# Performance work log

Hardware: AMD Instinct MI355X
Metric: run time of the kernel (lower is better)

The kernel has to match this reference:

```python
import jax, jax.numpy as jnp
import numpy as np
from jax import lax

NUM_CLASSES = 80
LAMBDA_BOX = 5.0   # lambda_coord
LAMBDA_OBJ = 1.0
LAMBDA_CLS = 1.0
SIMOTA_TOPK = 10
EPS = 1e-8


def _pairwise_iou(a, b):
    # a: [G,4], b: [N,4], boxes in x1,y1,x2,y2 -> [G,N]
    lt = jnp.maximum(a[:, None, :2], b[None, :, :2])
    rb = jnp.minimum(a[:, None, 2:], b[None, :, 2:])
    wh = jnp.clip(rb - lt, 0.0)
    inter = wh[..., 0] * wh[..., 1]
    area_a = jnp.clip(a[:, 2] - a[:, 0], 0.0) * jnp.clip(a[:, 3] - a[:, 1], 0.0)
    area_b = jnp.clip(b[:, 2] - b[:, 0], 0.0) * jnp.clip(b[:, 3] - b[:, 1], 0.0)
    return inter / (area_a[:, None] + area_b[None, :] - inter + EPS)


def _elem_iou(a, b):
    # a, b: [N,4] -> [N]
    lt = jnp.maximum(a[:, :2], b[:, :2])
    rb = jnp.minimum(a[:, 2:], b[:, 2:])
    wh = jnp.clip(rb - lt, 0.0)
    inter = wh[:, 0] * wh[:, 1]
    area_a = jnp.clip(a[:, 2] - a[:, 0], 0.0) * jnp.clip(a[:, 3] - a[:, 1], 0.0)
    area_b = jnp.clip(b[:, 2] - b[:, 0], 0.0) * jnp.clip(b[:, 3] - b[:, 1], 0.0)
    return inter / (area_a + area_b - inter + EPS)


def _bce_logits(x, y):
    # elementwise BCEWithLogits: softplus(x) - x*y  (== max(x,0)-x*y+log(1+exp(-|x|)))
    return jax.nn.softplus(x) - x * y


def _per_image(pred, gt_boxes, gt_labels):
    # pred: [N, 5+C]; gt_boxes: [G,4]; gt_labels: [G]
    N = pred.shape[0]
    G = gt_boxes.shape[0]
    C = NUM_CLASSES
    boxes_pred = pred[:, :4]
    obj_pred = pred[:, 4]
    cls_pred = pred[:, 5:]

    # ---- SimOTA matching (YOLOX-style) ----
    ious = _pairwise_iou(gt_boxes, boxes_pred)                 # [G,N]
    onehot = jax.nn.one_hot(gt_labels, C, dtype=pred.dtype)    # [G,C]
    # pairwise BCE cls cost: sum_c softplus(x_nc) - sum_c x_nc * y_gc
    sp_sum = jax.nn.softplus(cls_pred).sum(-1)                 # [N]
    pair_cls = sp_sum[None, :] - onehot @ cls_pred.T           # [G,N]
    cost = pair_cls + 3.0 * (-jnp.log(ious + EPS))             # [G,N]

    topk_ious, _ = lax.top_k(ious, SIMOTA_TOPK)                # [G,10]
    dynamic_ks = jnp.clip(topk_ious.sum(-1), 1.0, None).astype(jnp.int32)  # [G]

    # rank of each anchor in ascending cost order per gt
    ranks = jnp.argsort(jnp.argsort(cost, axis=1), axis=1)     # [G,N]
    matching = ranks < dynamic_ks[:, None]                     # [G,N] bool

    # conflict resolution: anchors matched to >1 gt keep only min-cost gt
    multi = matching.sum(0) > 1                                # [N]
    best_gt = jnp.argmin(cost, axis=0)                         # [N]
    keep = jax.nn.one_hot(best_gt, G, dtype=bool).T            # [G,N]
    matching = jnp.where(multi[None, :], matching & keep, matching)

    fg_mask = matching.any(0)                                  # [N]
    matched_gt_inds = matching.argmax(0)                       # [N]

    # ---- losses (means over fg, computed with masks) ----
    fg_f = fg_mask.astype(pred.dtype)
    nfg = jnp.maximum(fg_f.sum(), 1.0)

    agt_boxes = gt_boxes[matched_gt_inds]                      # [N,4]
    agt_labels = gt_labels[matched_gt_inds]                    # [N]

    d = boxes_pred - agt_boxes
    ad = jnp.abs(d)
    sl1 = jnp.where(ad < 1.0, 0.5 * d * d, ad - 0.5)
    box_loss = (sl1 * fg_f[:, None]).sum() / (nfg * 4.0)

    iou_t = lax.stop_gradient(_elem_iou(boxes_pred, agt_boxes))  # [N]
    obj_s = jax.nn.sigmoid(obj_pred)                             # note: original applies sigmoid then BCEWithLogits
    obj_loss = (_bce_logits(obj_s, iou_t) * fg_f).sum() / nfg

    cls_t = jax.nn.one_hot(agt_labels, C, dtype=pred.dtype)
    cls_loss = (_bce_logits(cls_pred, cls_t) * fg_f[:, None]).sum() / (nfg * C)

    return box_loss, obj_loss, cls_loss


def setup_inputs() -> dict:
    key = jax.random.key(0)
    k1, k2, k3 = jax.random.split(key, 3)
    B, A, H, W = 16, 3, 128, 128
    G = 60
    preds = jax.random.normal(k1, (B, A, H, W, 5 + NUM_CLASSES), dtype=jnp.float32)
    r = jax.random.uniform(k2, (B, G, 4), dtype=jnp.float32)
    xy = r[..., :2] * 100.0
    wh = r[..., 2:] * 20.0 + 1.0
    gt_boxes = jnp.concatenate([xy, xy + wh], axis=-1)
    gt_labels = jax.random.randint(k3, (B, G), 0, NUM_CLASSES, dtype=jnp.int32)
    return {"preds": preds, "gt_boxes": gt_boxes, "gt_labels": gt_labels}


def reference(preds, gt_boxes, gt_labels):
    B, A, H, W, D = preds.shape
    pred = preds[:, 0].reshape(B, H * W, D)
    bl, ol, cl = jax.vmap(_per_image)(pred, gt_boxes, gt_labels)
    box_loss = bl.sum()
    obj_loss = ol.sum()
    cls_loss = cl.sum()
    total = (LAMBDA_BOX * box_loss + LAMBDA_OBJ * obj_loss + LAMBDA_CLS * cls_loss) / B
    return total, box_loss / B, obj_loss / B, cls_loss / B
```

## Files before the change

kernel.cpp:

```cpp
#include <hip/hip_runtime.h>
#include <math.h>

#define BN 16
#define NA 16384
#define NG 60
#define NC 80
#define ND 85

__device__ __forceinline__ float softplusf(float x){
  return log1pf(expf(-fabsf(x))) + fmaxf(x, 0.0f);
}

__global__ __launch_bounds__(256) void k_prep(const float* __restrict__ preds,
    const int* __restrict__ gt_labels, float4* __restrict__ bx,
    float* __restrict__ spsum, float* __restrict__ objp, float* __restrict__ clsg)
{
  __shared__ float4 tilev[64*ND/4];
  __shared__ int lab[NG];
  __shared__ float psum[256];
  float* tile = (float*)tilev;
  const int t = threadIdx.x;
  const int blk = blockIdx.x;
  const int b = blk >> 8;
  const int n0 = (blk & 255) << 6;
  const float4* srcv = (const float4*)(preds + ((size_t)b*3*NA + n0)*ND);
  for (int i = t; i < 1360; i += 256) tilev[i] = srcv[i];
  if (t < NG) lab[t] = gt_labels[b*NG + t];
  __syncthreads();
  const int a = t & 63, q = t >> 6;
  float p = 0.f;
  #pragma unroll
  for (int c = 0; c < 20; c++) p += softplusf(tile[a*ND + 5 + q*20 + c]);
  psum[t] = p;
  __syncthreads();
  const size_t nb = (size_t)b*NA + n0;
  if (t < 64){
    float sp = psum[t] + psum[64+t] + psum[128+t] + psum[192+t];
    spsum[nb + t] = sp;
    bx[nb + t] = make_float4(tile[t*ND+0], tile[t*ND+1], tile[t*ND+2], tile[t*ND+3]);
    objp[nb + t] = tile[t*ND+4];
  }
  #pragma unroll
  for (int r = 0; r < 15; r++){
    int g = q*15 + r;
    clsg[(((size_t)b*NG + g) << 14) + n0 + a] = tile[a*ND + 5 + lab[g]];
  }
}

__global__ __launch_bounds__(256) void k_select(const float* __restrict__ gt_boxes,
    const float4* __restrict__ bx, const float* __restrict__ spsum,
    const float* __restrict__ clsg, int* __restrict__ matched, int* __restrict__ cnt)
{
  const int bid = blockIdx.x;
  const int g = bid >> 4, b = bid & 15;
  const int t = threadIdx.x;
  const int lane = t & 63, w = t >> 6;
  const float* gtp = gt_boxes + (b*NG + g)*4;
  const float gx1 = gtp[0], gy1 = gtp[1], gx2 = gtp[2], gy2 = gtp[3];
  const float garea = fmaxf(gx2-gx1,0.f)*fmaxf(gy2-gy1,0.f);
  const size_t nb = (size_t)b*NA;
  const float* clsrow = clsg + (((size_t)b*NG + g) << 14);

  float il[10];
  float cl[10]; int ci[10];
  #pragma unroll
  for (int j=0;j<10;j++){ il[j] = -1.f; cl[j] = INFINITY; ci[j] = 0x7fffffff; }

  for (int i = t; i < NA; i += 256){
    float4 bb = bx[nb + i];
    float parea = fmaxf(bb.z-bb.x,0.f)*fmaxf(bb.w-bb.y,0.f);
    float ix = fmaxf(fminf(gx2,bb.z)-fmaxf(gx1,bb.x), 0.f);
    float iy = fmaxf(fminf(gy2,bb.w)-fmaxf(gy1,bb.y), 0.f);
    float inter = ix*iy;
    float iou = inter/(garea + parea - inter + 1e-8f);
    float cost = spsum[nb+i] - clsrow[i] + 3.0f*(-logf(iou + 1e-8f));
    if (__any(iou > il[9])){
      float v = iou;
      #pragma unroll
      for (int j=0;j<10;j++){ bool c = v > il[j]; float o = il[j]; il[j]=c?v:o; v=c?o:v; }
    }
    if (__any((cost < cl[9]) || (cost == cl[9] && i < ci[9]))){
      float cv = cost; int ca = i;
      #pragma unroll
      for (int j=0;j<10;j++){
        bool c = (cv < cl[j]) || (cv == cl[j] && ca < ci[j]);
        float ov = cl[j]; int oa = ci[j];
        cl[j] = c?cv:ov; ci[j] = c?ca:oa;
        cv = c?ov:cv;    ca = c?oa:ca;
      }
    }
  }

  __shared__ float wv[4]; __shared__ int wa[4]; __shared__ int ww[4];
  __shared__ float bs10; __shared__ int bwin; __shared__ int bk;

  float s10 = 0.f;
  for (int r = 0; r < 10; r++){
    float v = il[0]; int who = t;
    #pragma unroll
    for (int off = 32; off; off >>= 1){
      float ov = __shfl_xor(v, off);
      int   ow = __shfl_xor(who, off);
      if (ov > v || (ov == v && ow < who)){ v = ov; who = ow; }
    }
    if (lane == 0){ wv[w] = v; ww[w] = who; }
    __syncthreads();
    if (t == 0){
      float bv = wv[0]; int bw = ww[0];
      for (int u=1; u<4; u++) if (wv[u] > bv || (wv[u]==bv && ww[u]<bw)){ bv=wv[u]; bw=ww[u]; }
      s10 += bv; bwin = bw;
    }
    __syncthreads();
    if (t == bwin){
      #pragma unroll
      for (int j=0;j<9;j++) il[j] = il[j+1];
      il[9] = -1.f;
    }
    __syncthreads();
  }
  if (t == 0) bk = (int)fmaxf(s10, 1.0f);
  __syncthreads();
  const int k = bk;

  for (int r = 0; r < k; r++){
    float v = cl[0]; int a = ci[0]; int who = t;
    #pragma unroll
    for (int off = 32; off; off >>= 1){
      float ov = __shfl_xor(v, off);
      int   oa = __shfl_xor(a, off);
      int   ow = __shfl_xor(who, off);
      if (ov < v || (ov == v && (oa < a || (oa == a && ow < who)))){ v=ov; a=oa; who=ow; }
    }
    if (lane == 0){ wv[w] = v; wa[w] = a; ww[w] = who; }
    __syncthreads();
    if (t == 0){
      float bv = wv[0]; int ba = wa[0]; int bw = ww[0];
      for (int u=1; u<4; u++) if (wv[u] < bv || (wv[u]==bv && wa[u] < ba)){ bv=wv[u]; ba=wa[u]; bw=ww[u]; }
      matched[bid*10 + r] = ba; bwin = bw;
    }
    __syncthreads();
    if (t == bwin){
      #pragma unroll
      for (int j=0;j<9;j++){ cl[j] = cl[j+1]; ci[j] = ci[j+1]; }
      cl[9] = INFINITY; ci[9] = 0x7fffffff;
    }
    __syncthreads();
  }
  if (t == 0) cnt[bid] = k;
}

__device__ __forceinline__ float blockSum(float v, float* red, int t){
  red[t] = v; __syncthreads();
  #pragma unroll
  for (int s = 128; s > 0; s >>= 1){
    if (t < s) red[t] += red[t+s];
    __syncthreads();
  }
  float r = red[0]; __syncthreads();
  return r;
}

__global__ __launch_bounds__(256) void k_loss(const float* __restrict__ gt_boxes,
    const int* __restrict__ matched, const int* __restrict__ cnt,
    const float4* __restrict__ bx, const float* __restrict__ spsum,
    const float* __restrict__ objp, const float* __restrict__ clsg,
    float* __restrict__ partials)
{
  __shared__ int lists[NG*10];
  __shared__ int cnts[NG];
  __shared__ float gtb[NG][4];
  __shared__ float red[256];
  const int b = blockIdx.x;
  const int t = threadIdx.x;
  for (int i = t; i < NG*10; i += 256){
    int g = i/10, j = i - g*10;
    lists[i] = matched[(g*16 + b)*10 + j];
  }
  if (t < NG){
    cnts[t] = cnt[t*16 + b];
    float4 gg = ((const float4*)gt_boxes)[b*NG + t];
    gtb[t][0]=gg.x; gtb[t][1]=gg.y; gtb[t][2]=gg.z; gtb[t][3]=gg.w;
  }
  __syncthreads();
  for (int i = t; i < NG*10; i += 256){
    int g = i/10, j = i - g*10;
    if (j >= cnts[g]) lists[i] = -1;
  }
  __syncthreads();

  float boxs = 0.f, objs = 0.f, clss = 0.f, nfg = 0.f;
  const size_t nb = (size_t)b*NA;
  for (int s = t; s < NG*10; s += 256){
    int n = lists[s];
    if (n < 0) continue;
    int g = s/10;
    int m = 0, firstg = -1;
    for (int gp = 0; gp < NG; gp++){
      bool mem = false;
      #pragma unroll
      for (int jp = 0; jp < 10; jp++) mem |= (lists[gp*10 + jp] == n);
      if (mem){ m++; if (firstg < 0) firstg = gp; }
    }
    if (g != firstg) continue;
    float4 bb = bx[nb + n];
    float sp = spsum[nb + n];
    int mg = g;
    if (m > 1){
      float parea = fmaxf(bb.z-bb.x,0.f)*fmaxf(bb.w-bb.y,0.f);
      float best = INFINITY; int bg = 0;
      for (int gp = 0; gp < NG; gp++){
        float ga = fmaxf(gtb[gp][2]-gtb[gp][0],0.f)*fmaxf(gtb[gp][3]-gtb[gp][1],0.f);
        float ix = fmaxf(fminf(gtb[gp][2],bb.z)-fmaxf(gtb[gp][0],bb.x),0.f);
        float iy = fmaxf(fminf(gtb[gp][3],bb.w)-fmaxf(gtb[gp][1],bb.y),0.f);
        float inter = ix*iy;
        float iou = inter/(ga + parea - inter + 1e-8f);
        float c = sp - clsg[(((size_t)b*NG + gp) << 14) + n] + 3.0f*(-logf(iou + 1e-8f));
        if (c < best){ best = c; bg = gp; }
      }
      bool mem = false;
      #pragma unroll
      for (int jp = 0; jp < 10; jp++) mem |= (lists[bg*10 + jp] == n);
      if (!mem) continue;
      mg = bg;
    }
    float gx1=gtb[mg][0], gy1=gtb[mg][1], gx2=gtb[mg][2], gy2=gtb[mg][3];
    float d0=bb.x-gx1, d1=bb.y-gy1, d2=bb.z-gx2, d3=bb.w-gy2;
    float a0=fabsf(d0), a1=fabsf(d1), a2=fabsf(d2), a3=fabsf(d3);
    float sl = (a0<1.f ? 0.5f*d0*d0 : a0-0.5f)
             + (a1<1.f ? 0.5f*d1*d1 : a1-0.5f)
             + (a2<1.f ? 0.5f*d2*d2 : a2-0.5f)
             + (a3<1.f ? 0.5f*d3*d3 : a3-0.5f);
    float parea = fmaxf(bb.z-bb.x,0.f)*fmaxf(bb.w-bb.y,0.f);
    float garea = fmaxf(gx2-gx1,0.f)*fmaxf(gy2-gy1,0.f);
    float ix = fmaxf(fminf(gx2,bb.z)-fmaxf(gx1,bb.x),0.f);
    float iy = fmaxf(fminf(gy2,bb.w)-fmaxf(gy1,bb.y),0.f);
    float inter = ix*iy;
    float iou_t = inter/(parea + garea - inter + 1e-8f);
    float ob = objp[nb + n];
    float sg = 1.f/(1.f + expf(-ob));
    float obce = softplusf(sg) - sg*iou_t;
    float clsb = sp - clsg[(((size_t)b*NG + mg) << 14) + n];
    boxs += sl; objs += obce; clss += clsb; nfg += 1.f;
  }
  float tb = blockSum(boxs, red, t);
  float to = blockSum(objs, red, t);
  float tc = blockSum(clss, red, t);
  float tn = blockSum(nfg,  red, t);
  if (t == 0){
    partials[b*4+0] = tb; partials[b*4+1] = to;
    partials[b*4+2] = tc; partials[b*4+3] = tn;
  }
}

__global__ void k_final(const float* __restrict__ partials, float* __restrict__ out){
  if (threadIdx.x == 0 && blockIdx.x == 0){
    float tb=0.f, to=0.f, tc=0.f;
    for (int b = 0; b < BN; b++){
      float nf = fmaxf(partials[b*4+3], 1.f);
      tb += partials[b*4+0] / (nf * 4.f);
      to += partials[b*4+1] / nf;
      tc += partials[b*4+2] / (nf * (float)NC);
    }
    out[0] = (5.f*tb + to + tc) / (float)BN;
    out[1] = tb / (float)BN;
    out[2] = to / (float)BN;
    out[3] = tc / (float)BN;
  }
}

extern "C" void kernel_launch(void* const* d_in, const int* in_sizes, int n_in,
                              void* d_out, int out_size, void* d_ws, size_t ws_size,
                              hipStream_t stream)
{
  (void)in_sizes; (void)n_in; (void)out_size; (void)ws_size;
  const float* preds     = (const float*)d_in[0];
  const float* gt_boxes  = (const float*)d_in[1];
  const int*   gt_labels = (const int*)d_in[2];
  float* out = (float*)d_out;

  char* ws = (char*)d_ws;
  float4* bx    = (float4*)ws;
  float*  spsum = (float*)(ws + (size_t)BN*NA*sizeof(float4));
  float*  objp  = spsum + (size_t)BN*NA;
  float*  clsg  = objp  + (size_t)BN*NA;
  int* matched  = (int*)(clsg + (size_t)BN*NG*NA);
  int* cnt      = matched + BN*NG*10;
  float* partials = (float*)(cnt + BN*NG);

  k_prep  <<<BN*NA/64, 256, 0, stream>>>(preds, gt_labels, bx, spsum, objp, clsg);
  k_select<<<BN*NG,    256, 0, stream>>>(gt_boxes, bx, spsum, clsg, matched, cnt);
  k_loss  <<<BN,       256, 0, stream>>>(gt_boxes, matched, cnt, bx, spsum, objp, clsg, partials);
  k_final <<<1, 64, 0, stream>>>(partials, out);
}
```

Baseline: 526.6 us.

## Fuse prep and selection into one tiled scan with per-slab top-k merge

Replaces the prep kernel, which materialised per-gt class logits (clsg, about 63 MB), and the per-gt selection kernel with one scan kernel. Each block loads a tile of anchors into shared memory once, computes softplus sums, and evaluates all 60 gts against it. It keeps per-thread top-10 IoU and cost lists, reduces them within 16-lane groups per slab, and a small merge kernel combines the slab candidates. The loss kernel now recomputes softplus sums and class logits directly from preds. Fast-math intrinsics replace the precise exp and log, and the tie-break on equal cost in the insertion is loosened, which may slightly change matching.

```diff
diff --git a/kernel.cpp b/kernel.cpp
--- a/kernel.cpp
+++ b/kernel.cpp
@@ -6,124 +6,185 @@
 #define NG 60
 #define NC 80
 #define ND 85
-
-__device__ __forceinline__ float softplusf(float x){
-  return log1pf(expf(-fabsf(x))) + fmaxf(x, 0.0f);
-}
-
-__global__ __launch_bounds__(256) void k_prep(const float* __restrict__ preds,
-    const int* __restrict__ gt_labels, float4* __restrict__ bx,
-    float* __restrict__ spsum, float* __restrict__ objp, float* __restrict__ clsg)
+#define SLABS 16
+#define SLAB 1024
+#define TILE 128
+#define NTILES 8
+#define GSLOT 64
+
+__device__ __forceinline__ float softplus_fast(float x){
+  return __logf(1.0f + __expf(-fabsf(x))) + fmaxf(x, 0.0f);
+}
+
+__global__ __launch_bounds__(1024) void f_scan(
+    const float* __restrict__ preds, const float* __restrict__ gt_boxes,
+    const int* __restrict__ gt_labels, float* __restrict__ mlist)
 {
-  __shared__ float4 tilev[64*ND/4];
-  __shared__ int lab[NG];
-  __shared__ float psum[256];
+  __shared__ float4 tilev[TILE*ND/4];
+  __shared__ float sp[TILE];
+  __shared__ float4 gtb4[GSLOT];
+  __shared__ float gar[GSLOT];
+  __shared__ int   lab[GSLOT];
   float* tile = (float*)tilev;
   const int t = threadIdx.x;
-  const int blk = blockIdx.x;
-  const int b = blk >> 8;
-  const int n0 = (blk & 255) << 6;
-  const float4* srcv = (const float4*)(preds + ((size_t)b*3*NA + n0)*ND);
-  for (int i = t; i < 1360; i += 256) tilev[i] = srcv[i];
-  if (t < NG) lab[t] = gt_labels[b*NG + t];
+  const int b = blockIdx.x >> 4;
+  const int slab = blockIdx.x & 15;
+
+  if (t < GSLOT){
+    float4 gg = make_float4(0.f,0.f,0.f,0.f);
+    int lb = 0;
+    if (t < NG){ gg = ((const float4*)gt_boxes)[b*NG + t]; lb = gt_labels[b*NG + t]; }
+    gtb4[t] = gg; lab[t] = lb;
+    gar[t] = fmaxf(gg.z-gg.x,0.f)*fmaxf(gg.w-gg.y,0.f);
+  }
   __syncthreads();
-  const int a = t & 63, q = t >> 6;
-  float p = 0.f;
-  #pragma unroll
-  for (int c = 0; c < 20; c++) p += softplusf(tile[a*ND + 5 + q*20 + c]);
-  psum[t] = p;
-  __syncthreads();
-  const size_t nb = (size_t)b*NA + n0;
-  if (t < 64){
-    float sp = psum[t] + psum[64+t] + psum[128+t] + psum[192+t];
-    spsum[nb + t] = sp;
-    bx[nb + t] = make_float4(tile[t*ND+0], tile[t*ND+1], tile[t*ND+2], tile[t*ND+3]);
-    objp[nb + t] = tile[t*ND+4];
-  }
-  #pragma unroll
-  for (int r = 0; r < 15; r++){
-    int g = q*15 + r;
-    clsg[(((size_t)b*NG + g) << 14) + n0 + a] = tile[a*ND + 5 + lab[g]];
-  }
-}
-
-__global__ __launch_bounds__(256) void k_select(const float* __restrict__ gt_boxes,
-    const float4* __restrict__ bx, const float* __restrict__ spsum,
-    const float* __restrict__ clsg, int* __restrict__ matched, int* __restrict__ cnt)
-{
-  const int bid = blockIdx.x;
-  const int g = bid >> 4, b = bid & 15;
-  const int t = threadIdx.x;
-  const int lane = t & 63, w = t >> 6;
-  const float* gtp = gt_boxes + (b*NG + g)*4;
-  const float gx1 = gtp[0], gy1 = gtp[1], gx2 = gtp[2], gy2 = gtp[3];
-  const float garea = fmaxf(gx2-gx1,0.f)*fmaxf(gy2-gy1,0.f);
-  const size_t nb = (size_t)b*NA;
-  const float* clsrow = clsg + (((size_t)b*NG + g) << 14);
-
-  float il[10];
-  float cl[10]; int ci[10];
+  const int g = t >> 4, strip = t & 15;
+  const float4 gt = gtb4[g];
+  const float ga = gar[g];
+  const int lg = lab[g];
+
+  float il[10], cl[10]; int ci[10];
   #pragma unroll
   for (int j=0;j<10;j++){ il[j] = -1.f; cl[j] = INFINITY; ci[j] = 0x7fffffff; }
 
-  for (int i = t; i < NA; i += 256){
-    float4 bb = bx[nb + i];
-    float parea = fmaxf(bb.z-bb.x,0.f)*fmaxf(bb.w-bb.y,0.f);
-    float ix = fmaxf(fminf(gx2,bb.z)-fmaxf(gx1,bb.x), 0.f);
-    float iy = fmaxf(fminf(gy2,bb.w)-fmaxf(gy1,bb.y), 0.f);
-    float inter = ix*iy;
-    float iou = inter/(garea + parea - inter + 1e-8f);
-    float cost = spsum[nb+i] - clsrow[i] + 3.0f*(-logf(iou + 1e-8f));
-    if (__any(iou > il[9])){
-      float v = iou;
-      #pragma unroll
-      for (int j=0;j<10;j++){ bool c = v > il[j]; float o = il[j]; il[j]=c?v:o; v=c?o:v; }
-    }
-    if (__any((cost < cl[9]) || (cost == cl[9] && i < ci[9]))){
-      float cv = cost; int ca = i;
-      #pragma unroll
-      for (int j=0;j<10;j++){
-        bool c = (cv < cl[j]) || (cv == cl[j] && ca < ci[j]);
-        float ov = cl[j]; int oa = ci[j];
-        cl[j] = c?cv:ov; ci[j] = c?ca:oa;
-        cv = c?ov:cv;    ca = c?oa:ca;
+  const float4* src0 = (const float4*)(preds + ((size_t)b*3*NA + (size_t)slab*SLAB)*ND);
+
+  for (int ti = 0; ti < NTILES; ti++){
+    __syncthreads();
+    const float4* src = src0 + (size_t)ti*(TILE*ND/4);
+    #pragma unroll
+    for (int i = 0; i < 3; i++){
+      int idx = t + i*1024;
+      if (idx < TILE*ND/4) tilev[idx] = src[idx];
+    }
+    __syncthreads();
+    {
+      int a = t >> 3, part = t & 7;
+      const float* rowc = tile + a*ND + 5 + part*10;
+      float p = 0.f;
+      #pragma unroll
+      for (int c = 0; c < 10; c++) p += softplus_fast(rowc[c]);
+      p += __shfl_xor(p, 1);
+      p += __shfl_xor(p, 2);
+      p += __shfl_xor(p, 4);
+      if (part == 0) sp[a] = p;
+    }
+    __syncthreads();
+    const int n0 = slab*SLAB + ti*TILE;
+    for (int r = 0; r < 8; r++){
+      int a = (r<<4) + strip;
+      const float* row = tile + a*ND;
+      float bx1=row[0], by1=row[1], bx2=row[2], by2=row[3];
+      float clsv = row[5+lg];
+      float spv  = sp[a];
+      float pa = fmaxf(bx2-bx1,0.f)*fmaxf(by2-by1,0.f);
+      float ix = fmaxf(fminf(gt.z,bx2)-fmaxf(gt.x,bx1),0.f);
+      float iy = fmaxf(fminf(gt.w,by2)-fmaxf(gt.y,by1),0.f);
+      float inter = ix*iy;
+      float iou = inter/(ga + pa - inter + 1e-8f);
+      float cost = fmaf(-3.0f, __logf(iou + 1e-8f), spv - clsv);
+      int idx = n0 + a;
+      if (__any(iou > il[9])){
+        float v = iou;
+        #pragma unroll
+        for (int j=0;j<10;j++){ bool c = v > il[j]; float o=il[j]; il[j]=c?v:o; v=c?o:v; }
       }
-    }
-  }
-
-  __shared__ float wv[4]; __shared__ int wa[4]; __shared__ int ww[4];
-  __shared__ float bs10; __shared__ int bwin; __shared__ int bk;
-
+      {
+        float cv = cost; int ca = idx;
+        #pragma unroll
+        for (int j=0;j<10;j++){
+          bool c = cv < cl[j];
+          float ov=cl[j]; int oa=ci[j];
+          cl[j]=c?cv:ov; ci[j]=c?ca:oa;
+          cv=c?ov:cv;    ca=c?oa:ca;
+        }
+      }
+    }
+  }
+
+  float* outp = mlist + (((size_t)(b*SLABS + slab))*NG + g)*30;
+  for (int r = 0; r < 10; r++){
+    float v = il[0]; int who = strip;
+    #pragma unroll
+    for (int off = 8; off; off >>= 1){
+      float ov = __shfl_xor(v, off, 16);
+      int   ow = __shfl_xor(who, off, 16);
+      if (ov > v || (ov == v && ow < who)){ v = ov; who = ow; }
+    }
+    if (strip == r && g < NG) outp[r] = v;
+    if (strip == who){
+      #pragma unroll
+      for (int j=0;j<9;j++) il[j] = il[j+1];
+      il[9] = -1.f;
+    }
+  }
+  for (int r = 0; r < 10; r++){
+    float v = cl[0]; int a = ci[0];
+    #pragma unroll
+    for (int off = 8; off; off >>= 1){
+      float ov = __shfl_xor(v, off, 16);
+      int   oa = __shfl_xor(a, off, 16);
+      if (ov < v || (ov == v && oa < a)){ v = ov; a = oa; }
+    }
+    if (strip == r && g < NG){ outp[10+r] = v; outp[20+r] = __int_as_float(a); }
+    if (cl[0] == v && ci[0] == a){
+      #pragma unroll
+      for (int j=0;j<9;j++){ cl[j]=cl[j+1]; ci[j]=ci[j+1]; }
+      cl[9] = INFINITY; ci[9] = 0x7fffffff;
+    }
+  }
+}
+
+__global__ __launch_bounds__(64) void f_merge(const float* __restrict__ mlist,
+    int* __restrict__ matched, int* __restrict__ cnt)
+{
+  __shared__ float buf[SLABS*30];
+  const int bid = blockIdx.x;
+  const int b = bid / NG, g = bid - b*NG;
+  const int t = threadIdx.x;
+  for (int i = t; i < SLABS*30; i += 64){
+    int slab = i / 30, j = i - slab*30;
+    buf[i] = mlist[(((size_t)(b*SLABS + slab))*NG + g)*30 + j];
+  }
+  __syncthreads();
+
+  float v0=-1.f, v1=-1.f, v2=-1.f;
+  {
+    int q0 = t, q1 = t+64, q2 = t+128;
+    v0 = buf[(q0/10)*30 + (q0%10)];
+    v1 = buf[(q1/10)*30 + (q1%10)];
+    if (q2 < 160) v2 = buf[(q2/10)*30 + (q2%10)];
+    if (v1 > v0){ float x=v0; v0=v1; v1=x; }
+    if (v2 > v1){ float x=v1; v1=v2; v2=x; }
+    if (v1 > v0){ float x=v0; v0=v1; v1=x; }
+  }
   float s10 = 0.f;
   for (int r = 0; r < 10; r++){
-    float v = il[0]; int who = t;
+    float v = v0; int who = t;
     #pragma unroll
     for (int off = 32; off; off >>= 1){
       float ov = __shfl_xor(v, off);
       int   ow = __shfl_xor(who, off);
       if (ov > v || (ov == v && ow < who)){ v = ov; who = ow; }
     }
-    if (lane == 0){ wv[w] = v; ww[w] = who; }
-    __syncthreads();
-    if (t == 0){
-      float bv = wv[0]; int bw = ww[0];
-      for (int u=1; u<4; u++) if (wv[u] > bv || (wv[u]==bv && ww[u]<bw)){ bv=wv[u]; bw=ww[u]; }
-      s10 += bv; bwin = bw;
-    }
-    __syncthreads();
-    if (t == bwin){
-      #pragma unroll
-      for (int j=0;j<9;j++) il[j] = il[j+1];
-      il[9] = -1.f;
-    }
-    __syncthreads();
-  }
-  if (t == 0) bk = (int)fmaxf(s10, 1.0f);
-  __syncthreads();
-  const int k = bk;
-
+    s10 += v;
+    if (t == who){ v0=v1; v1=v2; v2=-1.f; }
+  }
+  const int k = (int)fmaxf(s10, 1.0f);
+
+  float c0=INFINITY, c1=INFINITY, c2=INFINITY;
+  int   a0=0x7fffffff, a1=0x7fffffff, a2=0x7fffffff;
+  {
+    int q0 = t, q1 = t+64, q2 = t+128;
+    c0 = buf[(q0/10)*30 + 10 + (q0%10)]; a0 = __float_as_int(buf[(q0/10)*30 + 20 + (q0%10)]);
+    c1 = buf[(q1/10)*30 + 10 + (q1%10)]; a1 = __float_as_int(buf[(q1/10)*30 + 20 + (q1%10)]);
+    if (q2 < 160){ c2 = buf[(q2/10)*30 + 10 + (q2%10)]; a2 = __float_as_int(buf[(q2/10)*30 + 20 + (q2%10)]); }
+    if (c1 < c0 || (c1==c0 && a1 < a0)){ float x=c0;c0=c1;c1=x; int y=a0;a0=a1;a1=y; }
+    if (c2 < c1 || (c2==c1 && a2 < a1)){ float x=c1;c1=c2;c2=x; int y=a1;a1=a2;a2=y; }
+    if (c1 < c0 || (c1==c0 && a1 < a0)){ float x=c0;c0=c1;c1=x; int y=a0;a0=a1;a1=y; }
+  }
   for (int r = 0; r < k; r++){
-    float v = cl[0]; int a = ci[0]; int who = t;
+    float v = c0; int a = a0; int who = t;
     #pragma unroll
     for (int off = 32; off; off >>= 1){
       float ov = __shfl_xor(v, off);
@@ -131,20 +192,8 @@
       int   ow = __shfl_xor(who, off);
       if (ov < v || (ov == v && (oa < a || (oa == a && ow < who)))){ v=ov; a=oa; who=ow; }
     }
-    if (lane == 0){ wv[w] = v; wa[w] = a; ww[w] = who; }
-    __syncthreads();
-    if (t == 0){
-      float bv = wv[0]; int ba = wa[0]; int bw = ww[0];
-      for (int u=1; u<4; u++) if (wv[u] < bv || (wv[u]==bv && wa[u] < ba)){ bv=wv[u]; ba=wa[u]; bw=ww[u]; }
-      matched[bid*10 + r] = ba; bwin = bw;
-    }
-    __syncthreads();
-    if (t == bwin){
-      #pragma unroll
-      for (int j=0;j<9;j++){ cl[j] = cl[j+1]; ci[j] = ci[j+1]; }
-      cl[9] = INFINITY; ci[9] = 0x7fffffff;
-    }
-    __syncthreads();
+    if (t == r) matched[bid*10 + r] = a;
+    if (t == who){ c0=c1; a0=a1; c1=c2; a1=a2; c2=INFINITY; a2=0x7fffffff; }
   }
   if (t == 0) cnt[bid] = k;
 }
@@ -160,26 +209,24 @@
   return r;
 }
 
-__global__ __launch_bounds__(256) void k_loss(const float* __restrict__ gt_boxes,
+__global__ __launch_bounds__(256) void f_loss(const float* __restrict__ preds,
+    const float* __restrict__ gt_boxes, const int* __restrict__ gt_labels,
     const int* __restrict__ matched, const int* __restrict__ cnt,
-    const float4* __restrict__ bx, const float* __restrict__ spsum,
-    const float* __restrict__ objp, const float* __restrict__ clsg,
     float* __restrict__ partials)
 {
   __shared__ int lists[NG*10];
   __shared__ int cnts[NG];
   __shared__ float gtb[NG][4];
+  __shared__ int labs[NG];
   __shared__ float red[256];
   const int b = blockIdx.x;
   const int t = threadIdx.x;
-  for (int i = t; i < NG*10; i += 256){
-    int g = i/10, j = i - g*10;
-    lists[i] = matched[(g*16 + b)*10 + j];
-  }
+  for (int i = t; i < NG*10; i += 256) lists[i] = matched[b*NG*10 + i];
   if (t < NG){
-    cnts[t] = cnt[t*16 + b];
+    cnts[t] = cnt[b*NG + t];
     float4 gg = ((const float4*)gt_boxes)[b*NG + t];
     gtb[t][0]=gg.x; gtb[t][1]=gg.y; gtb[t][2]=gg.z; gtb[t][3]=gg.w;
+    labs[t] = gt_labels[b*NG + t];
   }
   __syncthreads();
   for (int i = t; i < NG*10; i += 256){
@@ -189,7 +236,7 @@
   __syncthreads();
 
   float boxs = 0.f, objs = 0.f, clss = 0.f, nfg = 0.f;
-  const size_t nb = (size_t)b*NA;
+  const float* rowb = preds + (size_t)b*3*NA*ND;
   for (int s = t; s < NG*10; s += 256){
     int n = lists[s];
     if (n < 0) continue;
@@ -202,19 +249,22 @@
       if (mem){ m++; if (firstg < 0) firstg = gp; }
     }
     if (g != firstg) continue;
-    float4 bb = bx[nb + n];
-    float sp = spsum[nb + n];
+    const float* row = rowb + (size_t)n*ND;
+    float p0=row[0], p1=row[1], p2=row[2], p3=row[3];
+    float obj = row[4];
+    float spv = 0.f;
+    for (int c = 0; c < NC; c++) spv += softplus_fast(row[5+c]);
     int mg = g;
+    float pa = fmaxf(p2-p0,0.f)*fmaxf(p3-p1,0.f);
     if (m > 1){
-      float parea = fmaxf(bb.z-bb.x,0.f)*fmaxf(bb.w-bb.y,0.f);
       float best = INFINITY; int bg = 0;
       for (int gp = 0; gp < NG; gp++){
         float ga = fmaxf(gtb[gp][2]-gtb[gp][0],0.f)*fmaxf(gtb[gp][3]-gtb[gp][1],0.f);
-        float ix = fmaxf(fminf(gtb[gp][2],bb.z)-fmaxf(gtb[gp][0],bb.x),0.f);
-        float iy = fmaxf(fminf(gtb[gp][3],bb.w)-fmaxf(gtb[gp][1],bb.y),0.f);
+        float ix = fmaxf(fminf(gtb[gp][2],p2)-fmaxf(gtb[gp][0],p0),0.f);
+        float iy = fmaxf(fminf(gtb[gp][3],p3)-fmaxf(gtb[gp][1],p1),0.f);
         float inter = ix*iy;
-        float iou = inter/(ga + parea - inter + 1e-8f);
-        float c = sp - clsg[(((size_t)b*NG + gp) << 14) + n] + 3.0f*(-logf(iou + 1e-8f));
+        float iou = inter/(ga + pa - inter + 1e-8f);
+        float c = fmaf(-3.0f, __logf(iou + 1e-8f), spv - row[5+labs[gp]]);
         if (c < best){ best = c; bg = gp; }
       }
       bool mem = false;
@@ -224,22 +274,20 @@
       mg = bg;
     }
     float gx1=gtb[mg][0], gy1=gtb[mg][1], gx2=gtb[mg][2], gy2=gtb[mg][3];
-    float d0=bb.x-gx1, d1=bb.y-gy1, d2=bb.z-gx2, d3=bb.w-gy2;
-    float a0=fabsf(d0), a1=fabsf(d1), a2=fabsf(d2), a3=fabsf(d3);
-    float sl = (a0<1.f ? 0.5f*d0*d0 : a0-0.5f)
-             + (a1<1.f ? 0.5f*d1*d1 : a1-0.5f)
-             + (a2<1.f ? 0.5f*d2*d2 : a2-0.5f)
-             + (a3<1.f ? 0.5f*d3*d3 : a3-0.5f);
-    float parea = fmaxf(bb.z-bb.x,0.f)*fmaxf(bb.w-bb.y,0.f);
-    float garea = fmaxf(gx2-gx1,0.f)*fmaxf(gy2-gy1,0.f);
-    float ix = fmaxf(fminf(gx2,bb.z)-fmaxf(gx1,bb.x),0.f);
-    float iy = fmaxf(fminf(gy2,bb.w)-fmaxf(gy1,bb.y),0.f);
+    float d0=p0-gx1, d1=p1-gy1, d2=p2-gx2, d3=p3-gy2;
+    float q0=fabsf(d0), q1=fabsf(d1), q2=fabsf(d2), q3=fabsf(d3);
+    float sl = (q0<1.f ? 0.5f*d0*d0 : q0-0.5f)
+             + (q1<1.f ? 0.5f*d1*d1 : q1-0.5f)
+             + (q2<1.f ? 0.5f*d2*d2 : q2-0.5f)
+             + (q3<1.f ? 0.5f*d3*d3 : q3-0.5f);
+    float ga = fmaxf(gx2-gx1,0.f)*fmaxf(gy2-gy1,0.f);
+    float ix = fmaxf(fminf(gx2,p2)-fmaxf(gx1,p0),0.f);
+    float iy = fmaxf(fminf(gy2,p3)-fmaxf(gy1,p1),0.f);
     float inter = ix*iy;
-    float iou_t = inter/(parea + garea - inter + 1e-8f);
-    float ob = objp[nb + n];
-    float sg = 1.f/(1.f + expf(-ob));
-    float obce = softplusf(sg) - sg*iou_t;
-    float clsb = sp - clsg[(((size_t)b*NG + mg) << 14) + n];
+    float iou_t = inter/(pa + ga - inter + 1e-8f);
+    float sg = 1.f/(1.f + __expf(-obj));
+    float obce = softplus_fast(sg) - sg*iou_t;
+    float clsb = spv - row[5+labs[mg]];
     boxs += sl; objs += obce; clss += clsb; nfg += 1.f;
   }
   float tb = blockSum(boxs, red, t);
@@ -252,7 +300,7 @@
   }
 }
 
-__global__ void k_final(const float* __restrict__ partials, float* __restrict__ out){
+__global__ void f_final(const float* __restrict__ partials, float* __restrict__ out){
   if (threadIdx.x == 0 && blockIdx.x == 0){
     float tb=0.f, to=0.f, tc=0.f;
     for (int b = 0; b < BN; b++){
@@ -278,17 +326,13 @@
   const int*   gt_labels = (const int*)d_in[2];
   float* out = (float*)d_out;
 
-  char* ws = (char*)d_ws;
-  float4* bx    = (float4*)ws;
-  float*  spsum = (float*)(ws + (size_t)BN*NA*sizeof(float4));
-  float*  objp  = spsum + (size_t)BN*NA;
-  float*  clsg  = objp  + (size_t)BN*NA;
-  int* matched  = (int*)(clsg + (size_t)BN*NG*NA);
+  float* mlist  = (float*)d_ws;
+  int* matched  = (int*)(mlist + (size_t)BN*SLABS*NG*30);
   int* cnt      = matched + BN*NG*10;
   float* partials = (float*)(cnt + BN*NG);
 
-  k_prep  <<<BN*NA/64, 256, 0, stream>>>(preds, gt_labels, bx, spsum, objp, clsg);
-  k_select<<<BN*NG,    256, 0, stream>>>(gt_boxes, bx, spsum, clsg, matched, cnt);
-  k_loss  <<<BN,       256, 0, stream>>>(gt_boxes, matched, cnt, bx, spsum, objp, clsg, partials);
-  k_final <<<1, 64, 0, stream>>>(partials, out);
-}
+  f_scan <<<BN*SLABS, 1024, 0, stream>>>(preds, gt_boxes, gt_labels, mlist);
+  f_merge<<<BN*NG,      64, 0, stream>>>(mlist, matched, cnt);
+  f_loss <<<BN,        256, 0, stream>>>(preds, gt_boxes, gt_labels, matched, cnt, partials);
+  f_final<<<1,          64, 0, stream>>>(partials, out);
+}
```

Result: faster. 498.4 us (-5.4%).
